# Kernel tuning notes

Measured on AMD Instinct MI355X. Metric: run time of the kernel, lower is better.

The kernel has to match this reference:

```python
import jax, jax.numpy as jnp
import numpy as np

D = 1024
H = 16
HD = D // H  # 64
BASE = 10000.0


def _rope_tables(seq_len, dtype=jnp.float32):
    # inv_freq over even dims, rotate-half convention: emb = cat(freqs, freqs)
    inv_freq = 1.0 / (BASE ** (jnp.arange(0, HD, 2, dtype=jnp.float32) / HD))
    t = jnp.arange(seq_len, dtype=jnp.float32)
    freqs = jnp.einsum('i,j->ij', t, inv_freq)          # [S, HD/2]
    emb = jnp.concatenate([freqs, freqs], axis=-1)       # [S, HD]
    return jnp.cos(emb).astype(dtype), jnp.sin(emb).astype(dtype)


def _rotate_half(x):
    x1, x2 = jnp.split(x, 2, axis=-1)
    return jnp.concatenate([-x2, x1], axis=-1)


def setup_inputs() -> dict:
    key = jax.random.key(0)
    ks = jax.random.split(key, 5)
    B, S = 2, 2048
    scale = 0.02
    return {
        'x': jax.random.normal(ks[0], (B, S, D), dtype=jnp.float32),
        'wq': jax.random.normal(ks[1], (D, D), dtype=jnp.float32) * scale,
        'wk': jax.random.normal(ks[2], (D, D), dtype=jnp.float32) * scale,
        'wv': jax.random.normal(ks[3], (D, D), dtype=jnp.float32) * scale,
        'wo': jax.random.normal(ks[4], (D, D), dtype=jnp.float32) * scale,
    }


def reference(x, wq, wk, wv, wo):
    B, S, _ = x.shape
    # QKV projections (torch Linear: x @ W^T), split into heads -> [B, H, S, HD]
    def proj(w):
        return jnp.einsum('bsd,ed->bse', x, w).reshape(B, S, H, HD).transpose(0, 2, 1, 3)
    q, k, v = proj(wq), proj(wk), proj(wv)

    # RoPE (rotate-half)
    cos, sin = _rope_tables(S, x.dtype)                  # [S, HD]
    cos = cos[None, None, :, :]
    sin = sin[None, None, :, :]
    q = q * cos + _rotate_half(q) * sin
    k = k * cos + _rotate_half(k) * sin

    # causal scaled-dot-product attention
    scores = jnp.einsum('bhqd,bhkd->bhqk', q, k) / jnp.sqrt(jnp.array(HD, x.dtype))
    causal = jnp.tril(jnp.ones((S, S), dtype=bool))
    scores = jnp.where(causal[None, None], scores, jnp.finfo(x.dtype).min)
    attn = jax.nn.softmax(scores, axis=-1)
    out = jnp.einsum('bhqk,bhkd->bhqd', attn, v)         # [B, H, S, HD]

    out = out.transpose(0, 2, 1, 3).reshape(B, S, D)
    return jnp.einsum('bsd,ed->bse', out, wo)
```

## Files before the change

### kernel.cpp

```cpp
#include <hip/hip_runtime.h>
#include <cstdint>
#include <cstddef>

typedef unsigned short u16;
typedef unsigned int u32;
typedef __bf16 bf16x8 __attribute__((ext_vector_type(8)));
typedef float f32x4 __attribute__((ext_vector_type(4)));
typedef u16 u16x8 __attribute__((ext_vector_type(8)));
typedef u16 u16x4 __attribute__((ext_vector_type(4)));

#define DD 1024
#define HH 16
#define HDIM 64
#define BB 2
#define SS 2048
#define MM (BB * SS)
#define NQT 32

__device__ __forceinline__ u16 cvt(float f) {
  __bf16 h = (__bf16)f;
  return __builtin_bit_cast(u16, h);
}
__device__ __forceinline__ f32x4 mfma16(bf16x8 a, bf16x8 b, f32x4 c) {
  return __builtin_amdgcn_mfma_f32_16x16x32_bf16(a, b, c, 0, 0, 0);
}
__device__ __forceinline__ bf16x8 ld_bf8(const u16* p) {
  return __builtin_bit_cast(bf16x8, *(const u16x8*)p);
}
__device__ __forceinline__ void async16(const void* g, void* l) {
  __builtin_amdgcn_global_load_lds(
      (__attribute__((address_space(1))) void*)(uintptr_t)g,
      (__attribute__((address_space(3))) void*)l, 16, 0, 0);
}

__global__ void cast_all(const float* __restrict__ x, const float* __restrict__ wq,
                         const float* __restrict__ wk, const float* __restrict__ wv,
                         const float* __restrict__ wo, u16* __restrict__ xb,
                         u16* __restrict__ wqb, u16* __restrict__ wkb,
                         u16* __restrict__ wvb, u16* __restrict__ wob) {
  int i = blockIdx.x * 256 + threadIdx.x;
  const float* src;
  u16* dst;
  int off;
  if (i < (1 << 20)) {
    src = x; dst = xb; off = i;
  } else {
    int j = i - (1 << 20);
    int w = j >> 18;
    off = j & ((1 << 18) - 1);
    src = (w == 0) ? wq : (w == 1) ? wk : (w == 2) ? wv : wo;
    dst = (w == 0) ? wqb : (w == 1) ? wkb : (w == 2) ? wvb : wob;
  }
  float4 v = ((const float4*)src)[off];
  u16x4 o;
  o[0] = cvt(v.x); o[1] = cvt(v.y); o[2] = cvt(v.z); o[3] = cvt(v.w);
  *(u16x4*)&dst[(size_t)off * 4] = o;
}

__global__ __launch_bounds__(256) void gemm_qkv(
    const u16* __restrict__ xb, const u16* __restrict__ wq,
    const u16* __restrict__ wk, const u16* __restrict__ wv,
    u16* __restrict__ Qo, u16* __restrict__ Ko, u16* __restrict__ Vto) {
  __shared__ __align__(16) u16 As[128 * 32];
  __shared__ __align__(16) u16 Bs[128 * 32];
  const int t = threadIdx.x;
  const int w = t >> 6, l = t & 63, lane16 = l & 15, quad = l >> 4;
  const int m0 = blockIdx.x * 128, n0 = blockIdx.y * 128;
  const u16* wsel = (blockIdx.z == 0) ? wq : (blockIdx.z == 1) ? wk : wv;
  const int m_w = (w >> 1) * 64, n_w = (w & 1) * 64;
  const int srow = t >> 2, scol = (t & 3) * 8;

  f32x4 acc[4][4] = {};
  for (int kt = 0; kt < 32; ++kt) {
    const int k0 = kt * 32;
    async16(&xb[(size_t)(m0 + srow) * DD + k0 + scol], &As[t * 8]);
    async16(&xb[(size_t)(m0 + 64 + srow) * DD + k0 + scol], &As[2048 + t * 8]);
    async16(&wsel[(size_t)(n0 + srow) * DD + k0 + scol], &Bs[t * 8]);
    async16(&wsel[(size_t)(n0 + 64 + srow) * DD + k0 + scol], &Bs[2048 + t * 8]);
    __syncthreads();
    bf16x8 af[4], bfr[4];
#pragma unroll
    for (int mi = 0; mi < 4; ++mi)
      af[mi] = ld_bf8(&As[(m_w + mi * 16 + lane16) * 32 + quad * 8]);
#pragma unroll
    for (int ni = 0; ni < 4; ++ni)
      bfr[ni] = ld_bf8(&Bs[(n_w + ni * 16 + lane16) * 32 + quad * 8]);
#pragma unroll
    for (int mi = 0; mi < 4; ++mi)
#pragma unroll
      for (int ni = 0; ni < 4; ++ni)
        acc[mi][ni] = mfma16(af[mi], bfr[ni], acc[mi][ni]);
    __syncthreads();
  }
  if (blockIdx.z == 2) {
#pragma unroll
    for (int mi = 0; mi < 4; ++mi) {
      int mbase = m0 + m_w + mi * 16 + quad * 4;
      int b = mbase >> 11, s0 = mbase & (SS - 1);
#pragma unroll
      for (int ni = 0; ni < 4; ++ni) {
        int e = n0 + n_w + ni * 16 + lane16;
        int h = e >> 6, d = e & 63;
        u16x4 pk;
#pragma unroll
        for (int r = 0; r < 4; ++r) pk[r] = cvt(acc[mi][ni][r]);
        *(u16x4*)&Vto[((size_t)(b * HH + h) * HDIM + d) * SS + s0] = pk;
      }
    }
  } else {
    u16* osel = (blockIdx.z == 0) ? Qo : Ko;
    const float scale = (blockIdx.z == 0) ? 0.18033688f : 1.0f;
    float invf[2];
    invf[0] = exp2f((float)lane16 * -0.4152410119f) * 0.15915494309f;
    invf[1] = exp2f((float)(16 + lane16) * -0.4152410119f) * 0.15915494309f;
    const int h = (n0 + n_w) >> 6;
#pragma unroll
    for (int mi = 0; mi < 4; ++mi) {
#pragma unroll
      for (int r = 0; r < 4; ++r) {
        int mrow = m0 + m_w + mi * 16 + quad * 4 + r;
        int b = mrow >> 11, s = mrow & (SS - 1);
        size_t rowbase = ((size_t)(b * HH + h) * SS + s) * HDIM;
#pragma unroll
        for (int ni = 0; ni < 2; ++ni) {
          float x1 = acc[mi][ni][r], x2 = acc[mi][ni + 2][r];
          float rv = (float)s * invf[ni];
          rv = rv - floorf(rv);
          float sn = __builtin_amdgcn_sinf(rv);
          float c  = __builtin_amdgcn_cosf(rv);
          int d = ni * 16 + lane16;
          osel[rowbase + d]      = cvt((x1 * c - x2 * sn) * scale);
          osel[rowbase + d + 32] = cvt((x2 * c + x1 * sn) * scale);
        }
      }
    }
  }
}

__global__ __launch_bounds__(256, 4) void attn_k(const u16* __restrict__ Qb,
                                                 const u16* __restrict__ Kb,
                                                 const u16* __restrict__ Vt,
                                                 u16* __restrict__ AO) {
  __shared__ __align__(16) u16 KsF[128 * 64];
  __shared__ __align__(16) u16 VtL[64 * 128];
  __shared__ __align__(16) u16 Ps[4][16 * 64];
  const int t = threadIdx.x;
  const int w = t >> 6, l = t & 63, lane16 = l & 15, quad = l >> 4;
  const int bh = blockIdx.x;
  const int jj = NQT - 1 - (int)blockIdx.y;
  const size_t base = (size_t)bh * SS * HDIM;
  const u16* Qp = Qb + base;
  const int b = bh >> 4, h = bh & 15;

  const int q0 = jj * 64;
  const int qrow = q0 + w * 16 + lane16;
  bf16x8 qf0 = ld_bf8(&Qp[(size_t)qrow * 64 + quad * 8]);
  bf16x8 qf1 = ld_bf8(&Qp[(size_t)qrow * 64 + 32 + quad * 8]);

  u16x8 onesu;
#pragma unroll
  for (int i = 0; i < 8; ++i) onesu[i] = 0x3F80;
  const bf16x8 ones = __builtin_bit_cast(bf16x8, onesu);

  f32x4 o[4] = {};
  f32x4 lacc = {};

  const u16* kptr[4];
  const u16* vptr[4];
#pragma unroll
  for (int i = 0; i < 4; ++i) {
    int p = i * 256 + t;
    int r = p >> 3;
    int c = (p & 7) ^ (r & 7);
    kptr[i] = Kb + base + (size_t)r * 64 + c * 8;
    int d = p >> 4;
    int q = (p & 15) ^ (d & 15);
    vptr[i] = Vt + base + (size_t)d * SS + q * 8;
  }

  u16* Pw = Ps[w];
  const int ktmax = jj >> 1;
  for (int kt = 0; kt <= ktmax; ++kt) {
    const int kv0 = kt * 128;
#pragma unroll
    for (int i = 0; i < 4; ++i) {
      async16(kptr[i], &KsF[(i * 256 + t) * 8]);
      kptr[i] += 128 * 64;
    }
#pragma unroll
    for (int i = 0; i < 4; ++i) {
      async16(vptr[i], &VtL[(i * 256 + t) * 8]);
      vptr[i] += 128;
    }
    __syncthreads();
    f32x4 st[8];
#pragma unroll
    for (int nc = 0; nc < 8; ++nc) {
      int rr = nc * 16 + lane16;
      int p0 = rr * 8 + (quad ^ (rr & 7));
      int p1 = rr * 8 + ((4 + quad) ^ (rr & 7));
      f32x4 a = {0.f, 0.f, 0.f, 0.f};
      a = mfma16(ld_bf8(&KsF[p0 * 8]), qf0, a);
      a = mfma16(ld_bf8(&KsF[p1 * 8]), qf1, a);
      st[nc] = a;
    }
    if (kt == ktmax) {
#pragma unroll
      for (int nc = 0; nc < 8; ++nc) {
        int kvb = kv0 + nc * 16 + quad * 4;
#pragma unroll
        for (int r = 0; r < 4; ++r)
          if (kvb + r > qrow) st[nc][r] = -3.0e38f;
      }
    }
#pragma unroll
    for (int nc = 0; nc < 8; ++nc)
#pragma unroll
      for (int r = 0; r < 4; ++r) st[nc][r] = exp2f(st[nc][r]);
#pragma unroll
    for (int kh = 0; kh < 2; ++kh) {
#pragma unroll
      for (int ncr = 0; ncr < 4; ++ncr) {
        f32x4 v = st[kh * 4 + ncr];
        u16x4 pk;
#pragma unroll
        for (int r = 0; r < 4; ++r) pk[r] = cvt(v[r]);
        int addr = lane16 * 64 + (((ncr * 2 + (quad >> 1)) ^ (lane16 & 7)) * 8) +
                   (quad & 1) * 4;
        *(u16x4*)&Pw[addr] = pk;
      }
#pragma unroll
      for (int cf = 0; cf < 2; ++cf) {
        bf16x8 pf = ld_bf8(&Pw[lane16 * 64 + (((cf * 4 + quad) ^ (lane16 & 7)) * 8)]);
        lacc = mfma16(ones, pf, lacc);
        int g = kh * 8 + cf * 4 + quad;
#pragma unroll
        for (int nd = 0; nd < 4; ++nd) {
          int d = nd * 16 + lane16;
          bf16x8 bv = ld_bf8(&VtL[(size_t)d * 128 + ((g ^ lane16) * 8)]);
          o[nd] = mfma16(bv, pf, o[nd]);
        }
      }
    }
    __syncthreads();
  }
  const float inv = 1.0f / lacc[0];
  const size_t rowb = (size_t)(b * SS + qrow) * DD + h * HDIM + quad * 4;
#pragma unroll
  for (int nd = 0; nd < 4; ++nd) {
    u16x4 pk;
#pragma unroll
    for (int r = 0; r < 4; ++r) pk[r] = cvt(o[nd][r] * inv);
    *(u16x4*)&AO[rowb + nd * 16] = pk;
  }
}

__global__ __launch_bounds__(256) void gemm_out(const u16* __restrict__ A, const u16* __restrict__ W,
                                                float* __restrict__ out) {
  __shared__ __align__(16) u16 As[128 * 32];
  __shared__ __align__(16) u16 Bs[128 * 32];
  const int t = threadIdx.x;
  const int w = t >> 6, l = t & 63, lane16 = l & 15, quad = l >> 4;
  const int m0 = blockIdx.x * 128, n0 = blockIdx.y * 128;
  const int m_w = (w >> 1) * 64, n_w = (w & 1) * 64;
  const int srow = t >> 2, scol = (t & 3) * 8;

  f32x4 acc[4][4] = {};
  for (int kt = 0; kt < 32; ++kt) {
    const int k0 = kt * 32;
    async16(&A[(size_t)(m0 + srow) * DD + k0 + scol], &As[t * 8]);
    async16(&A[(size_t)(m0 + 64 + srow) * DD + k0 + scol], &As[2048 + t * 8]);
    async16(&W[(size_t)(n0 + srow) * DD + k0 + scol], &Bs[t * 8]);
    async16(&W[(size_t)(n0 + 64 + srow) * DD + k0 + scol], &Bs[2048 + t * 8]);
    __syncthreads();
    bf16x8 af[4], bfr[4];
#pragma unroll
    for (int mi = 0; mi < 4; ++mi)
      af[mi] = ld_bf8(&As[(m_w + mi * 16 + lane16) * 32 + quad * 8]);
#pragma unroll
    for (int ni = 0; ni < 4; ++ni)
      bfr[ni] = ld_bf8(&Bs[(n_w + ni * 16 + lane16) * 32 + quad * 8]);
#pragma unroll
    for (int mi = 0; mi < 4; ++mi)
#pragma unroll
      for (int ni = 0; ni < 4; ++ni)
        acc[mi][ni] = mfma16(af[mi], bfr[ni], acc[mi][ni]);
    __syncthreads();
  }
#pragma unroll
  for (int mi = 0; mi < 4; ++mi) {
#pragma unroll
    for (int r = 0; r < 4; ++r) {
      int mrow = m0 + m_w + mi * 16 + quad * 4 + r;
#pragma unroll
      for (int ni = 0; ni < 4; ++ni) {
        int e = n0 + n_w + ni * 16 + lane16;
        out[(size_t)mrow * DD + e] = acc[mi][ni][r];
      }
    }
  }
}

extern "C" void kernel_launch(void* const* d_in, const int* in_sizes, int n_in,
                              void* d_out, int out_size, void* d_ws, size_t ws_size,
                              hipStream_t stream) {
  const float* x  = (const float*)d_in[0];
  const float* wq = (const float*)d_in[1];
  const float* wk = (const float*)d_in[2];
  const float* wv = (const float*)d_in[3];
  const float* wo = (const float*)d_in[4];
  float* out = (float*)d_out;
  char* ws = (char*)d_ws;

  u16* xb  = (u16*)(ws + (size_t)0);
  u16* wqb = (u16*)(ws + ((size_t)8  << 20));
  u16* wkb = (u16*)(ws + ((size_t)10 << 20));
  u16* wvb = (u16*)(ws + ((size_t)12 << 20));
  u16* wob = (u16*)(ws + ((size_t)14 << 20));
  u16* Qb  = (u16*)(ws + ((size_t)16 << 20));
  u16* Kb  = (u16*)(ws + ((size_t)24 << 20));
  u16* Vtg = (u16*)(ws + ((size_t)32 << 20));
  u16* AO  = (u16*)(ws + ((size_t)40 << 20));

  cast_all<<<8192, 256, 0, stream>>>(x, wq, wk, wv, wo, xb, wqb, wkb, wvb, wob);
  gemm_qkv<<<dim3(32, 8, 3), 256, 0, stream>>>(xb, wqb, wkb, wvb, Qb, Kb, Vtg);
  attn_k<<<dim3(32, 32), 256, 0, stream>>>(Qb, Kb, Vtg, AO);
  gemm_out<<<dim3(32, 8), 256, 0, stream>>>(AO, wob, out);
}
```

Baseline: 178.7 us.

## Double-buffer K/V tiles in attention and shrink output GEMM tile

```diff
diff --git a/kernel.cpp b/kernel.cpp
--- a/kernel.cpp
+++ b/kernel.cpp
@@ -137,13 +137,13 @@
   }
 }
 
-__global__ __launch_bounds__(256, 4) void attn_k(const u16* __restrict__ Qb,
+__global__ __launch_bounds__(256, 2) void attn_k(const u16* __restrict__ Qb,
                                                  const u16* __restrict__ Kb,
                                                  const u16* __restrict__ Vt,
                                                  u16* __restrict__ AO) {
-  __shared__ __align__(16) u16 KsF[128 * 64];
-  __shared__ __align__(16) u16 VtL[64 * 128];
-  __shared__ __align__(16) u16 Ps[4][16 * 64];
+  __shared__ __align__(16) u16 KsF[2][128 * 64];
+  __shared__ __align__(16) u16 VtL[2][64 * 128];
+  __shared__ __align__(16) u16 Ps[4][16 * 128];
   const int t = threadIdx.x;
   const int w = t >> 6, l = t & 63, lane16 = l & 15, quad = l >> 4;
   const int bh = blockIdx.x;
@@ -178,21 +178,31 @@
     vptr[i] = Vt + base + (size_t)d * SS + q * 8;
   }
 
+#pragma unroll
+  for (int i = 0; i < 4; ++i) {
+    async16(kptr[i], &KsF[0][(i * 256 + t) * 8]);
+    kptr[i] += 128 * 64;
+    async16(vptr[i], &VtL[0][(i * 256 + t) * 8]);
+    vptr[i] += 128;
+  }
+
   u16* Pw = Ps[w];
   const int ktmax = jj >> 1;
   for (int kt = 0; kt <= ktmax; ++kt) {
+    __syncthreads();
+    if (kt < ktmax) {
+      const int nb = (kt + 1) & 1;
+#pragma unroll
+      for (int i = 0; i < 4; ++i) {
+        async16(kptr[i], &KsF[nb][(i * 256 + t) * 8]);
+        kptr[i] += 128 * 64;
+        async16(vptr[i], &VtL[nb][(i * 256 + t) * 8]);
+        vptr[i] += 128;
+      }
+    }
+    const u16* Kc = KsF[kt & 1];
+    const u16* Vc = VtL[kt & 1];
     const int kv0 = kt * 128;
-#pragma unroll
-    for (int i = 0; i < 4; ++i) {
-      async16(kptr[i], &KsF[(i * 256 + t) * 8]);
-      kptr[i] += 128 * 64;
-    }
-#pragma unroll
-    for (int i = 0; i < 4; ++i) {
-      async16(vptr[i], &VtL[(i * 256 + t) * 8]);
-      vptr[i] += 128;
-    }
-    __syncthreads();
     f32x4 st[8];
 #pragma unroll
     for (int nc = 0; nc < 8; ++nc) {
@@ -200,8 +210,8 @@
       int p0 = rr * 8 + (quad ^ (rr & 7));
       int p1 = rr * 8 + ((4 + quad) ^ (rr & 7));
       f32x4 a = {0.f, 0.f, 0.f, 0.f};
-      a = mfma16(ld_bf8(&KsF[p0 * 8]), qf0, a);
-      a = mfma16(ld_bf8(&KsF[p1 * 8]), qf1, a);
+      a = mfma16(ld_bf8(&Kc[p0 * 8]), qf0, a);
+      a = mfma16(ld_bf8(&Kc[p1 * 8]), qf1, a);
       st[nc] = a;
     }
     if (kt == ktmax) {
@@ -218,31 +228,25 @@
 #pragma unroll
       for (int r = 0; r < 4; ++r) st[nc][r] = exp2f(st[nc][r]);
 #pragma unroll
-    for (int kh = 0; kh < 2; ++kh) {
-#pragma unroll
-      for (int ncr = 0; ncr < 4; ++ncr) {
-        f32x4 v = st[kh * 4 + ncr];
-        u16x4 pk;
-#pragma unroll
-        for (int r = 0; r < 4; ++r) pk[r] = cvt(v[r]);
-        int addr = lane16 * 64 + (((ncr * 2 + (quad >> 1)) ^ (lane16 & 7)) * 8) +
-                   (quad & 1) * 4;
-        *(u16x4*)&Pw[addr] = pk;
-      }
-#pragma unroll
-      for (int cf = 0; cf < 2; ++cf) {
-        bf16x8 pf = ld_bf8(&Pw[lane16 * 64 + (((cf * 4 + quad) ^ (lane16 & 7)) * 8)]);
-        lacc = mfma16(ones, pf, lacc);
-        int g = kh * 8 + cf * 4 + quad;
-#pragma unroll
-        for (int nd = 0; nd < 4; ++nd) {
-          int d = nd * 16 + lane16;
-          bf16x8 bv = ld_bf8(&VtL[(size_t)d * 128 + ((g ^ lane16) * 8)]);
-          o[nd] = mfma16(bv, pf, o[nd]);
-        }
-      }
-    }
-    __syncthreads();
+    for (int nc = 0; nc < 8; ++nc) {
+      u16x4 pk;
+#pragma unroll
+      for (int r = 0; r < 4; ++r) pk[r] = cvt(st[nc][r]);
+      int addr = lane16 * 128 + (((nc * 2 + (quad >> 1)) ^ lane16) * 8) + (quad & 1) * 4;
+      *(u16x4*)&Pw[addr] = pk;
+    }
+#pragma unroll
+    for (int G = 0; G < 4; ++G) {
+      int gc = ((G * 4 + quad) ^ lane16) * 8;
+      bf16x8 pf = ld_bf8(&Pw[lane16 * 128 + gc]);
+      lacc = mfma16(ones, pf, lacc);
+#pragma unroll
+      for (int nd = 0; nd < 4; ++nd) {
+        int d = nd * 16 + lane16;
+        bf16x8 bv = ld_bf8(&Vc[(size_t)d * 128 + gc]);
+        o[nd] = mfma16(bv, pf, o[nd]);
+      }
+    }
   }
   const float inv = 1.0f / lacc[0];
   const size_t rowb = (size_t)(b * SS + qrow) * DD + h * HDIM + quad * 4;
@@ -258,32 +262,31 @@
 __global__ __launch_bounds__(256) void gemm_out(const u16* __restrict__ A, const u16* __restrict__ W,
                                                 float* __restrict__ out) {
   __shared__ __align__(16) u16 As[128 * 32];
-  __shared__ __align__(16) u16 Bs[128 * 32];
+  __shared__ __align__(16) u16 Bs[64 * 32];
   const int t = threadIdx.x;
   const int w = t >> 6, l = t & 63, lane16 = l & 15, quad = l >> 4;
-  const int m0 = blockIdx.x * 128, n0 = blockIdx.y * 128;
-  const int m_w = (w >> 1) * 64, n_w = (w & 1) * 64;
+  const int m0 = blockIdx.x * 128, n0 = blockIdx.y * 64;
+  const int m_w = (w >> 1) * 64, n_w = (w & 1) * 32;
   const int srow = t >> 2, scol = (t & 3) * 8;
 
-  f32x4 acc[4][4] = {};
+  f32x4 acc[4][2] = {};
   for (int kt = 0; kt < 32; ++kt) {
     const int k0 = kt * 32;
     async16(&A[(size_t)(m0 + srow) * DD + k0 + scol], &As[t * 8]);
     async16(&A[(size_t)(m0 + 64 + srow) * DD + k0 + scol], &As[2048 + t * 8]);
     async16(&W[(size_t)(n0 + srow) * DD + k0 + scol], &Bs[t * 8]);
-    async16(&W[(size_t)(n0 + 64 + srow) * DD + k0 + scol], &Bs[2048 + t * 8]);
-    __syncthreads();
-    bf16x8 af[4], bfr[4];
+    __syncthreads();
+    bf16x8 af[4], bfr[2];
 #pragma unroll
     for (int mi = 0; mi < 4; ++mi)
       af[mi] = ld_bf8(&As[(m_w + mi * 16 + lane16) * 32 + quad * 8]);
 #pragma unroll
-    for (int ni = 0; ni < 4; ++ni)
+    for (int ni = 0; ni < 2; ++ni)
       bfr[ni] = ld_bf8(&Bs[(n_w + ni * 16 + lane16) * 32 + quad * 8]);
 #pragma unroll
     for (int mi = 0; mi < 4; ++mi)
 #pragma unroll
-      for (int ni = 0; ni < 4; ++ni)
+      for (int ni = 0; ni < 2; ++ni)
         acc[mi][ni] = mfma16(af[mi], bfr[ni], acc[mi][ni]);
     __syncthreads();
   }
@@ -293,7 +296,7 @@
     for (int r = 0; r < 4; ++r) {
       int mrow = m0 + m_w + mi * 16 + quad * 4 + r;
 #pragma unroll
-      for (int ni = 0; ni < 4; ++ni) {
+      for (int ni = 0; ni < 2; ++ni) {
         int e = n0 + n_w + ni * 16 + lane16;
         out[(size_t)mrow * DD + e] = acc[mi][ni][r];
       }
@@ -325,5 +328,5 @@
   cast_all<<<8192, 256, 0, stream>>>(x, wq, wk, wv, wo, xb, wqb, wkb, wvb, wob);
   gemm_qkv<<<dim3(32, 8, 3), 256, 0, stream>>>(xb, wqb, wkb, wvb, Qb, Kb, Vtg);
   attn_k<<<dim3(32, 32), 256, 0, stream>>>(Qb, Kb, Vtg, AO);
-  gemm_out<<<dim3(32, 8), 256, 0, stream>>>(AO, wob, out);
-}
+  gemm_out<<<dim3(32, 16), 256, 0, stream>>>(AO, wob, out);
+}
```

After: 168.5 us. 5.7% less time.

## Double GEMM K-tile to 64 with XOR-swizzled LDS, halve out-GEMM N tile

Applied to the files above, without the earlier changes.

```diff
diff --git a/kernel.cpp b/kernel.cpp
--- a/kernel.cpp
+++ b/kernel.cpp
@@ -61,35 +61,50 @@
     const u16* __restrict__ xb, const u16* __restrict__ wq,
     const u16* __restrict__ wk, const u16* __restrict__ wv,
     u16* __restrict__ Qo, u16* __restrict__ Ko, u16* __restrict__ Vto) {
-  __shared__ __align__(16) u16 As[128 * 32];
-  __shared__ __align__(16) u16 Bs[128 * 32];
+  __shared__ __align__(16) u16 As[128 * 64];
+  __shared__ __align__(16) u16 Bs[128 * 64];
   const int t = threadIdx.x;
   const int w = t >> 6, l = t & 63, lane16 = l & 15, quad = l >> 4;
   const int m0 = blockIdx.x * 128, n0 = blockIdx.y * 128;
   const u16* wsel = (blockIdx.z == 0) ? wq : (blockIdx.z == 1) ? wk : wv;
   const int m_w = (w >> 1) * 64, n_w = (w & 1) * 64;
-  const int srow = t >> 2, scol = (t & 3) * 8;
+
+  int srow[4], scol[4];
+#pragma unroll
+  for (int i = 0; i < 4; ++i) {
+    int p = i * 256 + t;
+    srow[i] = p >> 3;
+    scol[i] = ((p & 7) ^ (srow[i] & 7)) * 8;
+  }
 
   f32x4 acc[4][4] = {};
-  for (int kt = 0; kt < 32; ++kt) {
-    const int k0 = kt * 32;
-    async16(&xb[(size_t)(m0 + srow) * DD + k0 + scol], &As[t * 8]);
-    async16(&xb[(size_t)(m0 + 64 + srow) * DD + k0 + scol], &As[2048 + t * 8]);
-    async16(&wsel[(size_t)(n0 + srow) * DD + k0 + scol], &Bs[t * 8]);
-    async16(&wsel[(size_t)(n0 + 64 + srow) * DD + k0 + scol], &Bs[2048 + t * 8]);
-    __syncthreads();
-    bf16x8 af[4], bfr[4];
-#pragma unroll
-    for (int mi = 0; mi < 4; ++mi)
-      af[mi] = ld_bf8(&As[(m_w + mi * 16 + lane16) * 32 + quad * 8]);
-#pragma unroll
-    for (int ni = 0; ni < 4; ++ni)
-      bfr[ni] = ld_bf8(&Bs[(n_w + ni * 16 + lane16) * 32 + quad * 8]);
-#pragma unroll
-    for (int mi = 0; mi < 4; ++mi)
-#pragma unroll
-      for (int ni = 0; ni < 4; ++ni)
-        acc[mi][ni] = mfma16(af[mi], bfr[ni], acc[mi][ni]);
+  for (int kt = 0; kt < 16; ++kt) {
+    const int k0 = kt * 64;
+#pragma unroll
+    for (int i = 0; i < 4; ++i) {
+      async16(&xb[(size_t)(m0 + srow[i]) * DD + k0 + scol[i]], &As[(i * 256 + t) * 8]);
+      async16(&wsel[(size_t)(n0 + srow[i]) * DD + k0 + scol[i]], &Bs[(i * 256 + t) * 8]);
+    }
+    __syncthreads();
+#pragma unroll
+    for (int h = 0; h < 2; ++h) {
+      bf16x8 af[4], bfr[4];
+#pragma unroll
+      for (int mi = 0; mi < 4; ++mi) {
+        int rr = m_w + mi * 16 + lane16;
+        af[mi] = ld_bf8(&As[(rr * 8 + ((h * 4 + quad) ^ (rr & 7))) * 8]);
+      }
+#pragma unroll
+      for (int ni = 0; ni < 4; ++ni) {
+        int rr = n_w + ni * 16 + lane16;
+        bfr[ni] = ld_bf8(&Bs[(rr * 8 + ((h * 4 + quad) ^ (rr & 7))) * 8]);
+      }
+#pragma unroll
+      for (int mi = 0; mi < 4; ++mi)
+#pragma unroll
+        for (int ni = 0; ni < 4; ++ni)
+          acc[mi][ni] = mfma16(af[mi], bfr[ni], acc[mi][ni]);
+    }
     __syncthreads();
   }
   if (blockIdx.z == 2) {
@@ -186,9 +201,6 @@
     for (int i = 0; i < 4; ++i) {
       async16(kptr[i], &KsF[(i * 256 + t) * 8]);
       kptr[i] += 128 * 64;
-    }
-#pragma unroll
-    for (int i = 0; i < 4; ++i) {
       async16(vptr[i], &VtL[(i * 256 + t) * 8]);
       vptr[i] += 128;
     }
@@ -257,34 +269,53 @@
 
 __global__ __launch_bounds__(256) void gemm_out(const u16* __restrict__ A, const u16* __restrict__ W,
                                                 float* __restrict__ out) {
-  __shared__ __align__(16) u16 As[128 * 32];
-  __shared__ __align__(16) u16 Bs[128 * 32];
+  __shared__ __align__(16) u16 As[128 * 64];
+  __shared__ __align__(16) u16 Bs[64 * 64];
   const int t = threadIdx.x;
   const int w = t >> 6, l = t & 63, lane16 = l & 15, quad = l >> 4;
-  const int m0 = blockIdx.x * 128, n0 = blockIdx.y * 128;
-  const int m_w = (w >> 1) * 64, n_w = (w & 1) * 64;
-  const int srow = t >> 2, scol = (t & 3) * 8;
-
-  f32x4 acc[4][4] = {};
-  for (int kt = 0; kt < 32; ++kt) {
-    const int k0 = kt * 32;
-    async16(&A[(size_t)(m0 + srow) * DD + k0 + scol], &As[t * 8]);
-    async16(&A[(size_t)(m0 + 64 + srow) * DD + k0 + scol], &As[2048 + t * 8]);
-    async16(&W[(size_t)(n0 + srow) * DD + k0 + scol], &Bs[t * 8]);
-    async16(&W[(size_t)(n0 + 64 + srow) * DD + k0 + scol], &Bs[2048 + t * 8]);
-    __syncthreads();
-    bf16x8 af[4], bfr[4];
-#pragma unroll
-    for (int mi = 0; mi < 4; ++mi)
-      af[mi] = ld_bf8(&As[(m_w + mi * 16 + lane16) * 32 + quad * 8]);
-#pragma unroll
-    for (int ni = 0; ni < 4; ++ni)
-      bfr[ni] = ld_bf8(&Bs[(n_w + ni * 16 + lane16) * 32 + quad * 8]);
-#pragma unroll
-    for (int mi = 0; mi < 4; ++mi)
-#pragma unroll
-      for (int ni = 0; ni < 4; ++ni)
-        acc[mi][ni] = mfma16(af[mi], bfr[ni], acc[mi][ni]);
+  const int m0 = blockIdx.x * 128, n0 = blockIdx.y * 64;
+  const int m_w = (w >> 1) * 64, n_w = (w & 1) * 32;
+
+  int arow[4], acol[4];
+#pragma unroll
+  for (int i = 0; i < 4; ++i) {
+    int p = i * 256 + t;
+    arow[i] = p >> 3;
+    acol[i] = ((p & 7) ^ (arow[i] & 7)) * 8;
+  }
+  const int brow = (512 + t) >> 3 & 63;
+  int br0 = t >> 3,        bc0 = ((t & 7) ^ (br0 & 7)) * 8;
+  int br1 = (256 + t) >> 3, bc1 = (((256 + t) & 7) ^ (br1 & 7)) * 8;
+  (void)brow;
+
+  f32x4 acc[4][2] = {};
+  for (int kt = 0; kt < 16; ++kt) {
+    const int k0 = kt * 64;
+#pragma unroll
+    for (int i = 0; i < 4; ++i)
+      async16(&A[(size_t)(m0 + arow[i]) * DD + k0 + acol[i]], &As[(i * 256 + t) * 8]);
+    async16(&W[(size_t)(n0 + br0) * DD + k0 + bc0], &Bs[t * 8]);
+    async16(&W[(size_t)(n0 + br1) * DD + k0 + bc1], &Bs[(256 + t) * 8]);
+    __syncthreads();
+#pragma unroll
+    for (int h = 0; h < 2; ++h) {
+      bf16x8 af[4], bfr[2];
+#pragma unroll
+      for (int mi = 0; mi < 4; ++mi) {
+        int rr = m_w + mi * 16 + lane16;
+        af[mi] = ld_bf8(&As[(rr * 8 + ((h * 4 + quad) ^ (rr & 7))) * 8]);
+      }
+#pragma unroll
+      for (int ni = 0; ni < 2; ++ni) {
+        int rr = n_w + ni * 16 + lane16;
+        bfr[ni] = ld_bf8(&Bs[(rr * 8 + ((h * 4 + quad) ^ (rr & 7))) * 8]);
+      }
+#pragma unroll
+      for (int mi = 0; mi < 4; ++mi)
+#pragma unroll
+        for (int ni = 0; ni < 2; ++ni)
+          acc[mi][ni] = mfma16(af[mi], bfr[ni], acc[mi][ni]);
+    }
     __syncthreads();
   }
 #pragma unroll
@@ -293,7 +324,7 @@
     for (int r = 0; r < 4; ++r) {
       int mrow = m0 + m_w + mi * 16 + quad * 4 + r;
 #pragma unroll
-      for (int ni = 0; ni < 4; ++ni) {
+      for (int ni = 0; ni < 2; ++ni) {
         int e = n0 + n_w + ni * 16 + lane16;
         out[(size_t)mrow * DD + e] = acc[mi][ni][r];
       }
@@ -325,5 +356,5 @@
   cast_all<<<8192, 256, 0, stream>>>(x, wq, wk, wv, wo, xb, wqb, wkb, wvb, wob);
   gemm_qkv<<<dim3(32, 8, 3), 256, 0, stream>>>(xb, wqb, wkb, wvb, Qb, Kb, Vtg);
   attn_k<<<dim3(32, 32), 256, 0, stream>>>(Qb, Kb, Vtg, AO);
-  gemm_out<<<dim3(32, 8), 256, 0, stream>>>(AO, wob, out);
-}
+  gemm_out<<<dim3(32, 16), 256, 0, stream>>>(AO, wob, out);
+}
```

Measured after the change: 177.9 us. No clear change (-0.4%).
